# Kernel tuning notes

Measured on AMD Instinct MI355X. Metric: run time of the kernel, lower is better.

Reference implementation:

```python
import jax, jax.numpy as jnp
import numpy as np

EPS = 1e-5

def gamma_layer_norm(x, gamma):
    # LayerNorm over last dim with learnable gamma only (no bias)
    mu = jnp.mean(x, axis=-1, keepdims=True)
    var = jnp.var(x, axis=-1, keepdims=True)
    return (x - mu) * jax.lax.rsqrt(var + EPS) * gamma

def setup_inputs() -> dict:
    key = jax.random.key(0)
    k1, k2, k3, k4 = jax.random.split(key, 4)
    b, n, dim = 8, 4096, 512
    heads, head_size = 8, 64
    hidden = heads * head_size  # 512
    x = jax.random.normal(k1, (b, n, dim), dtype=jnp.float32)
    # nn.Linear(dim, hidden*3, bias=False): weight [3*hidden, dim]
    w_qkv = jax.random.normal(k2, (3 * hidden, dim), dtype=jnp.float32) * (dim ** -0.5)
    # nn.Linear(hidden, dim, bias=False): weight [dim, hidden]
    w_out = jax.random.normal(k3, (dim, hidden), dtype=jnp.float32) * (hidden ** -0.5)
    gamma = 1.0 + 0.02 * jax.random.normal(k4, (dim,), dtype=jnp.float32)
    return {"x": x, "w_qkv": w_qkv, "w_out": w_out, "gamma": gamma}

def reference(x, w_qkv, w_out, gamma):
    b, n, dim = x.shape
    heads, head_size = 8, 64
    scale = head_size ** -0.5
    # norm=False -> Identity; no time conditioning
    qkv = jnp.einsum('bnd,hd->bnh', x, w_qkv)  # [b, n, 3*hidden]
    q, k, v = jnp.split(qkv, 3, axis=-1)
    def to_heads(t):
        return t.reshape(b, n, heads, head_size).transpose(0, 2, 1, 3)  # b h n d
    q, k, v = to_heads(q), to_heads(k), to_heads(v)
    q = jax.nn.softmax(q, axis=-1) * scale   # softmax over feature dim
    k = jax.nn.softmax(k, axis=-2)           # softmax over sequence dim
    context = jnp.einsum('bhnd,bhne->bhde', k, v)      # [b, h, d, e]
    out = jnp.einsum('bhde,bhnd->bhne', context, q)    # [b, h, n, e]
    out = out.transpose(0, 2, 1, 3).reshape(b, n, heads * head_size)
    out = jnp.einsum('bnh,dh->bnd', out, w_out)
    out = gamma_layer_norm(out, gamma)  # dropout inactive (p=0 / eval)
    return out
```

## Files before the change

### kernel.cpp

```cpp
#include <hip/hip_runtime.h>
#include <hip/hip_bf16.h>
#include <stdint.h>
#include <stddef.h>

typedef __bf16 bf16_t;
typedef __bf16 bf16x8 __attribute__((ext_vector_type(8)));
typedef float floatx4 __attribute__((ext_vector_type(4)));

#define DIM 512
#define SEQ 4096
#define BATCH 8

static __device__ __forceinline__ floatx4 mfma_bf16(bf16x8 a, bf16x8 b, floatx4 c) {
  return __builtin_amdgcn_mfma_f32_16x16x32_bf16(a, b, c, 0, 0, 0);
}

typedef __attribute__((address_space(1))) const void* gas_ptr;
typedef __attribute__((address_space(3))) void* las_ptr;
static __device__ __forceinline__ void gll16(const void* g, void* l) {
  __builtin_amdgcn_global_load_lds((gas_ptr)g, (las_ptr)l, 16, 0, 0);
}

__global__ __launch_bounds__(256) void k_cvt(const float* __restrict__ w, bf16_t* __restrict__ wb) {
  int i = (blockIdx.x * 256 + threadIdx.x) * 8;
  float4 a = *(const float4*)&w[i];
  float4 b = *(const float4*)&w[i + 4];
  bf16x8 o;
  o[0] = (bf16_t)a.x; o[1] = (bf16_t)a.y; o[2] = (bf16_t)a.z; o[3] = (bf16_t)a.w;
  o[4] = (bf16_t)b.x; o[5] = (bf16_t)b.y; o[6] = (bf16_t)b.z; o[7] = (bf16_t)b.w;
  *(bf16x8*)&wb[i] = o;
}

__global__ __launch_bounds__(512, 2) void k_qkv(const bf16_t* __restrict__ Xb,
                                                const bf16_t* __restrict__ Wb,
                                                bf16_t* __restrict__ qs,
                                                bf16_t* __restrict__ ek,
                                                bf16_t* __restrict__ vb,
                                                float* __restrict__ S) {
  __shared__ __align__(16) bf16_t As[256 * 64];
  __shared__ __align__(16) bf16_t Bs[256 * 64];
  const int tid = threadIdx.x;
  const int lane = tid & 63;
  const int w = tid >> 6;
  const int wr = w >> 2, wc = w & 3;
  const int l15 = lane & 15, l4 = lane >> 4;
  const int m0 = blockIdx.x * 256;
  const int n0 = blockIdx.y * 256;

  const int srow = tid >> 3;
  const int sunit = (tid & 7) ^ (srow & 7);
  const bf16_t* gA = Xb + (size_t)(m0 + srow) * DIM + (sunit << 3);
  const bf16_t* gB = Wb + (size_t)(n0 + srow) * DIM + (sunit << 3);
  bf16_t* lA = As + tid * 8;
  bf16_t* lB = Bs + tid * 8;

  floatx4 acc[8][4];
#pragma unroll
  for (int i = 0; i < 8; ++i)
#pragma unroll
    for (int j = 0; j < 4; ++j) acc[i][j] = (floatx4){0.f, 0.f, 0.f, 0.f};

  for (int kt = 0; kt < DIM; kt += 64) {
#pragma unroll
    for (int i = 0; i < 4; ++i) {
      gll16(gA + (size_t)i * 64 * DIM, lA + i * 64 * 64);
      gll16(gB + (size_t)i * 64 * DIM, lB + i * 64 * 64);
    }
    gA += 64; gB += 64;
    __syncthreads();
#pragma unroll
    for (int kk = 0; kk < 2; ++kk) {
      bf16x8 af[8], bfr[4];
#pragma unroll
      for (int f = 0; f < 8; ++f) {
        int ar = wr * 128 + f * 16 + l15;
        int ua = (kk * 4 + l4) ^ (ar & 7);
        af[f] = *(const bf16x8*)(As + ar * 64 + ua * 8);
      }
#pragma unroll
      for (int f = 0; f < 4; ++f) {
        int br = wc * 64 + f * 16 + l15;
        int ub = (kk * 4 + l4) ^ (br & 7);
        bfr[f] = *(const bf16x8*)(Bs + br * 64 + ub * 8);
      }
#pragma unroll
      for (int i = 0; i < 8; ++i)
#pragma unroll
        for (int j = 0; j < 4; ++j)
          acc[i][j] = mfma_bf16(af[i], bfr[j], acc[i][j]);
    }
    __syncthreads();
  }

  const int colbase = n0 + wc * 64;
  if (n0 < 512) {
#pragma unroll
    for (int fm = 0; fm < 8; ++fm) {
#pragma unroll
      for (int r = 0; r < 4; ++r) {
        float v0 = acc[fm][0][r], v1 = acc[fm][1][r], v2 = acc[fm][2][r], v3 = acc[fm][3][r];
        float mx = fmaxf(fmaxf(v0, v1), fmaxf(v2, v3));
        mx = fmaxf(mx, __shfl_xor(mx, 1));
        mx = fmaxf(mx, __shfl_xor(mx, 2));
        mx = fmaxf(mx, __shfl_xor(mx, 4));
        mx = fmaxf(mx, __shfl_xor(mx, 8));
        float e0 = __expf(v0 - mx), e1 = __expf(v1 - mx), e2 = __expf(v2 - mx), e3 = __expf(v3 - mx);
        float s = e0 + e1 + e2 + e3;
        s += __shfl_xor(s, 1); s += __shfl_xor(s, 2); s += __shfl_xor(s, 4); s += __shfl_xor(s, 8);
        float inv = 0.125f / s;
        int m = m0 + wr * 128 + fm * 16 + l4 * 4 + r;
        bf16_t* rowp = qs + (size_t)m * DIM + colbase;
        rowp[l15]      = (bf16_t)(e0 * inv);
        rowp[16 + l15] = (bf16_t)(e1 * inv);
        rowp[32 + l15] = (bf16_t)(e2 * inv);
        rowp[48 + l15] = (bf16_t)(e3 * inv);
      }
    }
  } else if (n0 < 1024) {
    const int cb = colbase - 512;
    float c0 = 0.f, c1 = 0.f, c2 = 0.f, c3 = 0.f;
#pragma unroll
    for (int fm = 0; fm < 8; ++fm) {
#pragma unroll
      for (int r = 0; r < 4; ++r) {
        int m = m0 + wr * 128 + fm * 16 + l4 * 4 + r;
        bf16_t* rowp = ek + (size_t)m * DIM + cb;
        float e0 = __expf(acc[fm][0][r]);
        float e1 = __expf(acc[fm][1][r]);
        float e2 = __expf(acc[fm][2][r]);
        float e3 = __expf(acc[fm][3][r]);
        rowp[l15]      = (bf16_t)e0;
        rowp[16 + l15] = (bf16_t)e1;
        rowp[32 + l15] = (bf16_t)e2;
        rowp[48 + l15] = (bf16_t)e3;
        c0 += e0; c1 += e1; c2 += e2; c3 += e3;
      }
    }
    c0 += __shfl_xor(c0, 16); c0 += __shfl_xor(c0, 32);
    c1 += __shfl_xor(c1, 16); c1 += __shfl_xor(c1, 32);
    c2 += __shfl_xor(c2, 16); c2 += __shfl_xor(c2, 32);
    c3 += __shfl_xor(c3, 16); c3 += __shfl_xor(c3, 32);
    if (lane < 16) {
      int b = m0 >> 12;
      atomicAdd(&S[b * 512 + cb + lane],      c0);
      atomicAdd(&S[b * 512 + cb + 16 + lane], c1);
      atomicAdd(&S[b * 512 + cb + 32 + lane], c2);
      atomicAdd(&S[b * 512 + cb + 48 + lane], c3);
    }
  } else {
    const int cb = colbase - 1024;
#pragma unroll
    for (int fm = 0; fm < 8; ++fm) {
#pragma unroll
      for (int r = 0; r < 4; ++r) {
        int m = m0 + wr * 128 + fm * 16 + l4 * 4 + r;
        bf16_t* rowp = vb + (size_t)m * DIM + cb;
        rowp[l15]      = (bf16_t)acc[fm][0][r];
        rowp[16 + l15] = (bf16_t)acc[fm][1][r];
        rowp[32 + l15] = (bf16_t)acc[fm][2][r];
        rowp[48 + l15] = (bf16_t)acc[fm][3][r];
      }
    }
  }
}

#define TP 136
__global__ __launch_bounds__(256) void k_ctx(const bf16_t* __restrict__ ek,
                                             const bf16_t* __restrict__ vb,
                                             float* __restrict__ ctxpart) {
  __shared__ __align__(16) bf16_t ekT[64 * TP];
  __shared__ __align__(16) bf16_t vT[64 * TP];
  __shared__ float red[4096];
  const int tid = threadIdx.x;
  const int lane = tid & 63, wid = tid >> 6;
  const int l15 = lane & 15, l4 = lane >> 4;
  const int bh = blockIdx.x, chunk = blockIdx.y;
  const int b = bh >> 3, h = bh & 7;
  const int base = b * SEQ + chunk * 512;

  floatx4 acc[4][4];
#pragma unroll
  for (int i = 0; i < 4; ++i)
#pragma unroll
    for (int j = 0; j < 4; ++j) acc[i][j] = (floatx4){0.f, 0.f, 0.f, 0.f};

  for (int nt = 0; nt < 4; ++nt) {
    const int n0 = base + nt * 128;
#pragma unroll
    for (int i = 0; i < 4; ++i) {
      int q = tid + i * 256;
      int n = q & 127;
      int c8 = (q >> 7) << 3;
      bf16x8 vk = *(const bf16x8*)&ek[(size_t)(n0 + n) * DIM + h * 64 + c8];
      bf16x8 vv = *(const bf16x8*)&vb[(size_t)(n0 + n) * DIM + h * 64 + c8];
#pragma unroll
      for (int j = 0; j < 8; ++j) {
        ekT[(c8 + j) * TP + n] = vk[j];
        vT [(c8 + j) * TP + n] = vv[j];
      }
    }
    __syncthreads();
    const int nb = wid * 32;
    bf16x8 af[4], bfr[4];
#pragma unroll
    for (int f = 0; f < 4; ++f) {
      af[f]  = *(const bf16x8*)&ekT[(f * 16 + l15) * TP + nb + l4 * 8];
      bfr[f] = *(const bf16x8*)&vT [(f * 16 + l15) * TP + nb + l4 * 8];
    }
#pragma unroll
    for (int i = 0; i < 4; ++i)
#pragma unroll
      for (int j = 0; j < 4; ++j)
        acc[i][j] = mfma_bf16(af[i], bfr[j], acc[i][j]);
    __syncthreads();
  }

  for (int w = 0; w < 4; ++w) {
    if (wid == w) {
#pragma unroll
      for (int fm = 0; fm < 4; ++fm)
#pragma unroll
        for (int fn = 0; fn < 4; ++fn)
#pragma unroll
          for (int r = 0; r < 4; ++r) {
            int d = fm * 16 + l4 * 4 + r;
            int e = fn * 16 + l15;
            if (w == 0) red[d * 64 + e] = acc[fm][fn][r];
            else        red[d * 64 + e] += acc[fm][fn][r];
          }
    }
    __syncthreads();
  }
  float* dst = ctxpart + ((size_t)bh * 8 + chunk) * 4096;
#pragma unroll
  for (int i = 0; i < 4; ++i) {
    int q = tid + i * 256;
    *(float4*)&dst[q * 4] = *(const float4*)&red[q * 4];
  }
}

__global__ __launch_bounds__(256) void k_mt(const float* __restrict__ ctxpart,
                                            const float* __restrict__ S,
                                            const float* __restrict__ w_out,
                                            bf16_t* __restrict__ Mt) {
  __shared__ float cs[4096];
  const int tid = threadIdx.x;
  const int bh = blockIdx.x;
  const int b = bh >> 3, h = bh & 7;
#pragma unroll
  for (int i = 0; i < 16; ++i) {
    int idx = tid + i * 256;
    float s = 0.f;
#pragma unroll
    for (int p = 0; p < 8; ++p) s += ctxpart[((size_t)bh * 8 + p) * 4096 + idx];
    cs[idx] = s / S[b * 512 + h * 64 + (idx >> 6)];
  }
  __syncthreads();
  for (int half = 0; half < 2; ++half) {
    const int dcol = half * 256 + tid;
    float a[64];
#pragma unroll
    for (int d = 0; d < 64; ++d) a[d] = 0.f;
    for (int e = 0; e < 64; ++e) {
      float we = w_out[(size_t)dcol * 512 + h * 64 + e];
#pragma unroll
      for (int d = 0; d < 64; ++d) a[d] += cs[d * 64 + e] * we;
    }
    bf16_t* dst = Mt + ((size_t)b * 512 + dcol) * 512 + h * 64;
#pragma unroll
    for (int g = 0; g < 8; ++g) {
      bf16x8 o;
#pragma unroll
      for (int j = 0; j < 8; ++j) o[j] = (bf16_t)a[g * 8 + j];
      *(bf16x8*)&dst[g * 8] = o;
    }
  }
}

__global__ __launch_bounds__(512, 2) void k_out(const bf16_t* __restrict__ qs,
                                                const bf16_t* __restrict__ Mt,
                                                bf16_t* __restrict__ out2b) {
  __shared__ __align__(16) bf16_t As[256 * 64];
  __shared__ __align__(16) bf16_t Bs[256 * 64];
  const int tid = threadIdx.x;
  const int lane = tid & 63;
  const int w = tid >> 6;
  const int wr = w >> 2, wc = w & 3;
  const int l15 = lane & 15, l4 = lane >> 4;
  const int m0 = blockIdx.x * 256;
  const int n0 = blockIdx.y * 256;
  const bf16_t* Bp = Mt + (size_t)(blockIdx.x >> 4) * 512 * 512;

  const int srow = tid >> 3;
  const int sunit = (tid & 7) ^ (srow & 7);
  const bf16_t* gA = qs + (size_t)(m0 + srow) * 512 + (sunit << 3);
  const bf16_t* gB = Bp + (size_t)(n0 + srow) * 512 + (sunit << 3);
  bf16_t* lA = As + tid * 8;
  bf16_t* lB = Bs + tid * 8;

  floatx4 acc[8][4];
#pragma unroll
  for (int i = 0; i < 8; ++i)
#pragma unroll
    for (int j = 0; j < 4; ++j) acc[i][j] = (floatx4){0.f, 0.f, 0.f, 0.f};

  for (int kt = 0; kt < 512; kt += 64) {
#pragma unroll
    for (int i = 0; i < 4; ++i) {
      gll16(gA + (size_t)i * 64 * 512, lA + i * 64 * 64);
      gll16(gB + (size_t)i * 64 * 512, lB + i * 64 * 64);
    }
    gA += 64; gB += 64;
    __syncthreads();
#pragma unroll
    for (int kk = 0; kk < 2; ++kk) {
      bf16x8 af[8], bfr[4];
#pragma unroll
      for (int f = 0; f < 8; ++f) {
        int ar = wr * 128 + f * 16 + l15;
        int ua = (kk * 4 + l4) ^ (ar & 7);
        af[f] = *(const bf16x8*)(As + ar * 64 + ua * 8);
      }
#pragma unroll
      for (int f = 0; f < 4; ++f) {
        int br = wc * 64 + f * 16 + l15;
        int ub = (kk * 4 + l4) ^ (br & 7);
        bfr[f] = *(const bf16x8*)(Bs + br * 64 + ub * 8);
      }
#pragma unroll
      for (int i = 0; i < 8; ++i)
#pragma unroll
        for (int j = 0; j < 4; ++j)
          acc[i][j] = mfma_bf16(af[i], bfr[j], acc[i][j]);
    }
    __syncthreads();
  }
#pragma unroll
  for (int fm = 0; fm < 8; ++fm) {
#pragma unroll
    for (int r = 0; r < 4; ++r) {
      int m = m0 + wr * 128 + fm * 16 + l4 * 4 + r;
      bf16_t* rowp = out2b + (size_t)m * 512 + n0 + wc * 64;
      rowp[l15]      = (bf16_t)acc[fm][0][r];
      rowp[16 + l15] = (bf16_t)acc[fm][1][r];
      rowp[32 + l15] = (bf16_t)acc[fm][2][r];
      rowp[48 + l15] = (bf16_t)acc[fm][3][r];
    }
  }
}

__global__ __launch_bounds__(256) void k_ln(const bf16_t* __restrict__ out2b,
                                            const float* __restrict__ gamma,
                                            float* __restrict__ out) {
  const int lane = threadIdx.x & 63;
  const int row = blockIdx.x * 4 + (threadIdx.x >> 6);
  bf16x8 v = *(const bf16x8*)(out2b + (size_t)row * 512 + lane * 8);
  float f[8];
#pragma unroll
  for (int j = 0; j < 8; ++j) f[j] = (float)v[j];
  float s = 0.f, q = 0.f;
#pragma unroll
  for (int j = 0; j < 8; ++j) { s += f[j]; q += f[j] * f[j]; }
#pragma unroll
  for (int m = 1; m <= 32; m <<= 1) { s += __shfl_xor(s, m); q += __shfl_xor(q, m); }
  float mean = s * (1.f / 512.f);
  float var = q * (1.f / 512.f) - mean * mean;
  float rstd = rsqrtf(var + 1e-5f);
  float4 g0 = ((const float4*)gamma)[lane * 2];
  float4 g1 = ((const float4*)gamma)[lane * 2 + 1];
  float4 o0, o1;
  o0.x = (f[0] - mean) * rstd * g0.x;
  o0.y = (f[1] - mean) * rstd * g0.y;
  o0.z = (f[2] - mean) * rstd * g0.z;
  o0.w = (f[3] - mean) * rstd * g0.w;
  o1.x = (f[4] - mean) * rstd * g1.x;
  o1.y = (f[5] - mean) * rstd * g1.y;
  o1.z = (f[6] - mean) * rstd * g1.z;
  o1.w = (f[7] - mean) * rstd * g1.w;
  float* y = out + (size_t)row * 512;
  ((float4*)y)[lane * 2]     = o0;
  ((float4*)y)[lane * 2 + 1] = o1;
}

extern "C" void kernel_launch(void* const* d_in, const int* in_sizes, int n_in,
                              void* d_out, int out_size, void* d_ws, size_t ws_size,
                              hipStream_t stream) {
  const float* x     = (const float*)d_in[0];
  const float* w_qkv = (const float*)d_in[1];
  const float* w_out = (const float*)d_in[2];
  const float* gamma = (const float*)d_in[3];
  float* out = (float*)d_out;
  char* ws = (char*)d_ws;

  bf16_t* qs      = (bf16_t*)(ws);
  bf16_t* ek      = (bf16_t*)(ws + 33554432);
  bf16_t* vb      = (bf16_t*)(ws + 67108864);
  bf16_t* wqkvb   = (bf16_t*)(ws + 100663296);
  float*  S       = (float*)(ws + 102236160);
  bf16_t* Xb      = (bf16_t*)(ws + 102252544);
  float*  ctxpart = (float*)(ws + 103301120);
  bf16_t* Mt      = (bf16_t*)(ws + 111689728);
  bf16_t* out2b   = (bf16_t*)(ws + 33554432);

  hipMemsetAsync(S, 0, BATCH * 512 * sizeof(float), stream);

  k_cvt<<<384, 256, 0, stream>>>(w_qkv, wqkvb);
  k_cvt<<<8192, 256, 0, stream>>>(x, Xb);

  dim3 g1(128, 6);
  k_qkv<<<g1, 512, 0, stream>>>(Xb, wqkvb, qs, ek, vb, S);

  dim3 g2(64, 8);
  k_ctx<<<g2, 256, 0, stream>>>(ek, vb, ctxpart);

  k_mt<<<64, 256, 0, stream>>>(ctxpart, S, w_out, Mt);

  dim3 g5(128, 2);
  k_out<<<g5, 512, 0, stream>>>(qs, Mt, out2b);

  k_ln<<<8192, 256, 0, stream>>>(out2b, gamma, out);
}
```

Baseline: 219.9 us.

## Fuse layer norm into output GEMM epilogue with full-row tiles

The output GEMM now computes full 512-column rows per block (128 rows x 512 cols, K-step 32) so the layer norm can run in the epilogue. Row sums and sums of squares are reduced across lanes with shuffles and across waves through shared memory, and the normalized fp32 result is written directly. This removes the bf16 intermediate round trip and the separate LN launch. Launch bounds rise to 4 blocks per SM for k_qkv and k_out, which may force register spills or cut the tile reuse per K step, and the grid shrinks to 256 blocks.

```diff
diff --git a/kernel.cpp b/kernel.cpp
--- a/kernel.cpp
+++ b/kernel.cpp
@@ -31,7 +31,7 @@
   *(bf16x8*)&wb[i] = o;
 }
 
-__global__ __launch_bounds__(512, 2) void k_qkv(const bf16_t* __restrict__ Xb,
+__global__ __launch_bounds__(512, 4) void k_qkv(const bf16_t* __restrict__ Xb,
                                                 const bf16_t* __restrict__ Wb,
                                                 bf16_t* __restrict__ qs,
                                                 bf16_t* __restrict__ ek,
@@ -277,109 +277,113 @@
   }
 }
 
-__global__ __launch_bounds__(512, 2) void k_out(const bf16_t* __restrict__ qs,
+__global__ __launch_bounds__(512, 4) void k_out(const bf16_t* __restrict__ qs,
                                                 const bf16_t* __restrict__ Mt,
-                                                bf16_t* __restrict__ out2b) {
-  __shared__ __align__(16) bf16_t As[256 * 64];
-  __shared__ __align__(16) bf16_t Bs[256 * 64];
+                                                const float* __restrict__ gamma,
+                                                float* __restrict__ out) {
+  __shared__ __align__(16) bf16_t As[128 * 32];
+  __shared__ __align__(16) bf16_t Bs[512 * 32];
+  __shared__ float redS[128 * 4];
+  __shared__ float redQ[128 * 4];
   const int tid = threadIdx.x;
   const int lane = tid & 63;
   const int w = tid >> 6;
   const int wr = w >> 2, wc = w & 3;
   const int l15 = lane & 15, l4 = lane >> 4;
-  const int m0 = blockIdx.x * 256;
-  const int n0 = blockIdx.y * 256;
-  const bf16_t* Bp = Mt + (size_t)(blockIdx.x >> 4) * 512 * 512;
-
-  const int srow = tid >> 3;
-  const int sunit = (tid & 7) ^ (srow & 7);
-  const bf16_t* gA = qs + (size_t)(m0 + srow) * 512 + (sunit << 3);
-  const bf16_t* gB = Bp + (size_t)(n0 + srow) * 512 + (sunit << 3);
+  const int m0 = blockIdx.x * 128;
+  const bf16_t* Bp = Mt + (size_t)(blockIdx.x >> 5) * 512 * 512;
+
+  {
+  }
+  const int ra = tid >> 2;
+  const int ua = (tid & 3) ^ (ra & 3) ^ ((ra >> 2) & 3);
+  const bf16_t* gA = qs + (size_t)(m0 + ra) * 512 + (ua << 3);
   bf16_t* lA = As + tid * 8;
-  bf16_t* lB = Bs + tid * 8;
-
-  floatx4 acc[8][4];
-#pragma unroll
-  for (int i = 0; i < 8; ++i)
-#pragma unroll
-    for (int j = 0; j < 4; ++j) acc[i][j] = (floatx4){0.f, 0.f, 0.f, 0.f};
-
-  for (int kt = 0; kt < 512; kt += 64) {
-#pragma unroll
-    for (int i = 0; i < 4; ++i) {
-      gll16(gA + (size_t)i * 64 * 512, lA + i * 64 * 64);
-      gll16(gB + (size_t)i * 64 * 512, lB + i * 64 * 64);
-    }
-    gA += 64; gB += 64;
-    __syncthreads();
-#pragma unroll
-    for (int kk = 0; kk < 2; ++kk) {
-      bf16x8 af[8], bfr[4];
-#pragma unroll
-      for (int f = 0; f < 8; ++f) {
-        int ar = wr * 128 + f * 16 + l15;
-        int ua = (kk * 4 + l4) ^ (ar & 7);
-        af[f] = *(const bf16x8*)(As + ar * 64 + ua * 8);
-      }
-#pragma unroll
-      for (int f = 0; f < 4; ++f) {
-        int br = wc * 64 + f * 16 + l15;
-        int ub = (kk * 4 + l4) ^ (br & 7);
-        bfr[f] = *(const bf16x8*)(Bs + br * 64 + ub * 8);
-      }
-#pragma unroll
-      for (int i = 0; i < 8; ++i)
-#pragma unroll
-        for (int j = 0; j < 4; ++j)
-          acc[i][j] = mfma_bf16(af[i], bfr[j], acc[i][j]);
-    }
-    __syncthreads();
-  }
-#pragma unroll
-  for (int fm = 0; fm < 8; ++fm) {
+  const bf16_t* gBt[4];
+  bf16_t* lBt[4];
+#pragma unroll
+  for (int i = 0; i < 4; ++i) {
+    int rb = (tid >> 2) + i * 128;
+    int ub = (tid & 3) ^ (rb & 3) ^ ((rb >> 2) & 3);
+    gBt[i] = Bp + (size_t)rb * 512 + (ub << 3);
+    lBt[i] = Bs + (tid + i * 512) * 8;
+  }
+
+  floatx4 acc[4][8];
+#pragma unroll
+  for (int i = 0; i < 4; ++i)
+#pragma unroll
+    for (int j = 0; j < 8; ++j) acc[i][j] = (floatx4){0.f, 0.f, 0.f, 0.f};
+
+  for (int kt = 0; kt < 512; kt += 32) {
+    gll16(gA + kt, lA);
+#pragma unroll
+    for (int i = 0; i < 4; ++i) gll16(gBt[i] + kt, lBt[i]);
+    __syncthreads();
+    bf16x8 af[4], bfr[8];
+#pragma unroll
+    for (int f = 0; f < 4; ++f) {
+      int ar = wr * 64 + f * 16 + l15;
+      int u = l4 ^ (ar & 3) ^ ((ar >> 2) & 3);
+      af[f] = *(const bf16x8*)(As + ar * 32 + u * 8);
+    }
+#pragma unroll
+    for (int f = 0; f < 8; ++f) {
+      int br = wc * 128 + f * 16 + l15;
+      int u = l4 ^ (br & 3) ^ ((br >> 2) & 3);
+      bfr[f] = *(const bf16x8*)(Bs + br * 32 + u * 8);
+    }
+#pragma unroll
+    for (int i = 0; i < 4; ++i)
+#pragma unroll
+      for (int j = 0; j < 8; ++j)
+        acc[i][j] = mfma_bf16(af[i], bfr[j], acc[i][j]);
+    __syncthreads();
+  }
+
+#pragma unroll
+  for (int fm = 0; fm < 4; ++fm) {
 #pragma unroll
     for (int r = 0; r < 4; ++r) {
-      int m = m0 + wr * 128 + fm * 16 + l4 * 4 + r;
-      bf16_t* rowp = out2b + (size_t)m * 512 + n0 + wc * 64;
-      rowp[l15]      = (bf16_t)acc[fm][0][r];
-      rowp[16 + l15] = (bf16_t)acc[fm][1][r];
-      rowp[32 + l15] = (bf16_t)acc[fm][2][r];
-      rowp[48 + l15] = (bf16_t)acc[fm][3][r];
-    }
-  }
-}
-
-__global__ __launch_bounds__(256) void k_ln(const bf16_t* __restrict__ out2b,
-                                            const float* __restrict__ gamma,
-                                            float* __restrict__ out) {
-  const int lane = threadIdx.x & 63;
-  const int row = blockIdx.x * 4 + (threadIdx.x >> 6);
-  bf16x8 v = *(const bf16x8*)(out2b + (size_t)row * 512 + lane * 8);
-  float f[8];
-#pragma unroll
-  for (int j = 0; j < 8; ++j) f[j] = (float)v[j];
-  float s = 0.f, q = 0.f;
-#pragma unroll
-  for (int j = 0; j < 8; ++j) { s += f[j]; q += f[j] * f[j]; }
-#pragma unroll
-  for (int m = 1; m <= 32; m <<= 1) { s += __shfl_xor(s, m); q += __shfl_xor(q, m); }
-  float mean = s * (1.f / 512.f);
-  float var = q * (1.f / 512.f) - mean * mean;
-  float rstd = rsqrtf(var + 1e-5f);
-  float4 g0 = ((const float4*)gamma)[lane * 2];
-  float4 g1 = ((const float4*)gamma)[lane * 2 + 1];
-  float4 o0, o1;
-  o0.x = (f[0] - mean) * rstd * g0.x;
-  o0.y = (f[1] - mean) * rstd * g0.y;
-  o0.z = (f[2] - mean) * rstd * g0.z;
-  o0.w = (f[3] - mean) * rstd * g0.w;
-  o1.x = (f[4] - mean) * rstd * g1.x;
-  o1.y = (f[5] - mean) * rstd * g1.y;
-  o1.z = (f[6] - mean) * rstd * g1.z;
-  o1.w = (f[7] - mean) * rstd * g1.w;
-  float* y = out + (size_t)row * 512;
-  ((float4*)y)[lane * 2]     = o0;
-  ((float4*)y)[lane * 2 + 1] = o1;
+      float s = 0.f, q = 0.f;
+#pragma unroll
+      for (int fn = 0; fn < 8; ++fn) {
+        float v = acc[fm][fn][r];
+        s += v; q += v * v;
+      }
+      s += __shfl_xor(s, 1); q += __shfl_xor(q, 1);
+      s += __shfl_xor(s, 2); q += __shfl_xor(q, 2);
+      s += __shfl_xor(s, 4); q += __shfl_xor(q, 4);
+      s += __shfl_xor(s, 8); q += __shfl_xor(q, 8);
+      if (l15 == 0) {
+        int rl = wr * 64 + fm * 16 + l4 * 4 + r;
+        redS[rl * 4 + wc] = s;
+        redQ[rl * 4 + wc] = q;
+      }
+    }
+  }
+  __syncthreads();
+  float gm[8];
+#pragma unroll
+  for (int fn = 0; fn < 8; ++fn) gm[fn] = gamma[wc * 128 + fn * 16 + l15];
+#pragma unroll
+  for (int fm = 0; fm < 4; ++fm) {
+#pragma unroll
+    for (int r = 0; r < 4; ++r) {
+      int rl = wr * 64 + fm * 16 + l4 * 4 + r;
+      float4 sv = *(const float4*)&redS[rl * 4];
+      float4 qv = *(const float4*)&redQ[rl * 4];
+      float S = sv.x + sv.y + sv.z + sv.w;
+      float Q = qv.x + qv.y + qv.z + qv.w;
+      float mean = S * (1.f / 512.f);
+      float var = Q * (1.f / 512.f) - mean * mean;
+      float rstd = rsqrtf(var + 1e-5f);
+      float* rowp = out + (size_t)(m0 + rl) * 512 + wc * 128 + l15;
+#pragma unroll
+      for (int fn = 0; fn < 8; ++fn)
+        rowp[fn * 16] = (acc[fm][fn][r] - mean) * rstd * gm[fn];
+    }
+  }
 }
 
 extern "C" void kernel_launch(void* const* d_in, const int* in_sizes, int n_in,
@@ -400,7 +404,6 @@
   bf16_t* Xb      = (bf16_t*)(ws + 102252544);
   float*  ctxpart = (float*)(ws + 103301120);
   bf16_t* Mt      = (bf16_t*)(ws + 111689728);
-  bf16_t* out2b   = (bf16_t*)(ws + 33554432);
 
   hipMemsetAsync(S, 0, BATCH * 512 * sizeof(float), stream);
 
@@ -415,8 +418,5 @@
 
   k_mt<<<64, 256, 0, stream>>>(ctxpart, S, w_out, Mt);
 
-  dim3 g5(128, 2);
-  k_out<<<g5, 512, 0, stream>>>(qs, Mt, out2b);
-
-  k_ln<<<8192, 256, 0, stream>>>(out2b, gamma, out);
-}
+  k_out<<<256, 512, 0, stream>>>(qs, Mt, gamma, out);
+}
```

After: 532.6 us. 2.42x slower.
